# Kernel optimization log

Hardware: AMD Instinct MI355X
Metric: run time of the kernel (lower is better)

Reference implementation:

```python
import jax, jax.numpy as jnp
import numpy as np

B, T, D, H = 8, 4096, 512, 64

def setup_inputs() -> dict:
    key = jax.random.key(0)
    ks = jax.random.split(key, 6)
    s = 0.02  # small init scale so exp(K), exp(wbias) stay numerically tame
    return {
        "x": jax.random.normal(ks[0], (B, T, D), dtype=jnp.float32),
        "wq": jax.random.normal(ks[1], (H, D), dtype=jnp.float32) * s,
        "bq": jnp.zeros((H,), dtype=jnp.float32),
        "wk": jax.random.normal(ks[2], (H, D), dtype=jnp.float32) * s,
        "bk": jnp.zeros((H,), dtype=jnp.float32),
        "wv": jax.random.normal(ks[3], (H, D), dtype=jnp.float32) * s,
        "bv": jnp.zeros((H,), dtype=jnp.float32),
        "wp": jax.random.normal(ks[4], (D, H), dtype=jnp.float32) * s,
        "bp": jnp.zeros((D,), dtype=jnp.float32),
        "wbias": jax.random.normal(ks[5], (T, T), dtype=jnp.float32) * s,
    }

def reference(x, wq, bq, wk, bk, wv, bv, wp, bp, wbias):
    # Q, K, V projections: [B, T, H]
    Q = jnp.einsum('btd,hd->bth', x, wq) + bq
    K = jnp.einsum('btd,hd->bth', x, wk) + bk
    V = jnp.einsum('btd,hd->bth', x, wv) + bv
    ew = jnp.exp(wbias)              # [T, T], computed once
    eK = jnp.exp(K)                  # [B, T, H]
    num = jnp.einsum('ts,bsh->bth', ew, eK * V)
    den = jnp.einsum('ts,bsh->bth', ew, eK)
    Yt = jax.nn.sigmoid(Q) * (num / den)
    # output projection back to dim: [B, T, D]
    return jnp.einsum('bth,dh->btd', Yt, wp) + bp
```

## Files before the change

kernel.cpp:

```cpp
#include <hip/hip_runtime.h>
#include <math.h>

typedef _Float16 f16;
typedef __attribute__((ext_vector_type(8))) _Float16 f16x8;
typedef __attribute__((ext_vector_type(4))) _Float16 f16x4;
typedef __attribute__((ext_vector_type(4))) float f32x4;
typedef __attribute__((ext_vector_type(16))) float f32x16;

#define MFMA16(a, b, c) __builtin_amdgcn_mfma_f32_16x16x32_f16((a), (b), (c), 0, 0, 0)
#define MFMA32(a, b, c) __builtin_amdgcn_mfma_f32_32x32x16_f16((a), (b), (c), 0, 0, 0)

__device__ __forceinline__ void gld16(const f16* g, f16* l) {
  __builtin_amdgcn_global_load_lds(
      (const __attribute__((address_space(1))) unsigned int*)g,
      (__attribute__((address_space(3))) unsigned int*)l, 16, 0, 0);
}

__device__ __forceinline__ f16x8 pack8(const float* src) {
  float4 f0 = *(const float4*)src;
  float4 f1 = *(const float4*)(src + 4);
  f16x8 v;
  v[0] = (f16)f0.x; v[1] = (f16)f0.y; v[2] = (f16)f0.z; v[3] = (f16)f0.w;
  v[4] = (f16)f1.x; v[5] = (f16)f1.y; v[6] = (f16)f1.z; v[7] = (f16)f1.w;
  return v;
}

__global__ __launch_bounds__(256) void prep_ew(const float* __restrict__ wb,
                                               f16* __restrict__ ew) {
  const size_t stride = (size_t)gridDim.x * 256;
  const size_t total = (size_t)4096 * 4096 / 4;
  for (size_t i = (size_t)blockIdx.x * 256 + threadIdx.x; i < total; i += stride) {
    float4 f = ((const float4*)wb)[i];
    f16x4 o;
    o.x = (f16)expf(f.x); o.y = (f16)expf(f.y);
    o.z = (f16)expf(f.z); o.w = (f16)expf(f.w);
    ((f16x4*)ew)[i] = o;
  }
}

__global__ __launch_bounds__(256) void prep_w(const float* __restrict__ wq,
                                              const float* __restrict__ wk,
                                              const float* __restrict__ wv,
                                              const float* __restrict__ wp,
                                              f16* __restrict__ wqkvb,
                                              f16* __restrict__ wpb) {
  int i = blockIdx.x * 256 + threadIdx.x;
  wqkvb[i] = (f16)wk[i];
  wqkvb[32768 + i] = (f16)wv[i];
  wqkvb[65536 + i] = (f16)wq[i];
  wpb[i] = (f16)wp[i];
}

__global__ __launch_bounds__(256) void k1_qkv(const float* __restrict__ x,
                                              const f16* __restrict__ wqkvb,
                                              const float* __restrict__ bq,
                                              const float* __restrict__ bk,
                                              const float* __restrict__ bv,
                                              f16* __restrict__ sigQ,
                                              f16* __restrict__ XT) {
  __shared__ alignas(16) f16 sW[192 * 64];
  __shared__ alignas(16) f16 sX[64 * 64];
  const int tid = threadIdx.x;
  const int wave = tid >> 6, lane = tid & 63;
  const int m0 = blockIdx.x * 64;
  const int l15 = lane & 15;

  f32x4 accQ[4], accK[4], accV[4];
#pragma unroll
  for (int j = 0; j < 4; ++j) {
    accQ[j] = (f32x4){0.f, 0.f, 0.f, 0.f};
    accK[j] = (f32x4){0.f, 0.f, 0.f, 0.f};
    accV[j] = (f32x4){0.f, 0.f, 0.f, 0.f};
  }

  const int sc8 = tid & 7;
  const int wr8 = (tid >> 3) & 7;
  const int wcol = (sc8 ^ wr8) * 8;

  for (int ks = 0; ks < 512; ks += 64) {
#pragma unroll
    for (int q = 0; q < 6; ++q) {
      int r = q * 32 + (tid >> 3);
      gld16(wqkvb + (size_t)r * 512 + ks + wcol, &sW[r * 64 + sc8 * 8]);
    }
#pragma unroll
    for (int u = 0; u < 2; ++u) {
      int un = tid + u * 256;
      int r = un >> 3, c8 = un & 7;
      *(f16x8*)&sX[r * 64 + ((c8 ^ (r & 7)) * 8)] =
          pack8(x + (size_t)(m0 + r) * 512 + ks + c8 * 8);
    }
    __syncthreads();
#pragma unroll
    for (int kk = 0; kk < 2; ++kk) {
      const int c = kk * 4 + (lane >> 4);
      const int rK = wave * 16 + l15;
      const int rV = 64 + rK;
      f16x8 aK = *(const f16x8*)&sW[rK * 64 + ((c ^ (rK & 7)) * 8)];
      f16x8 aV = *(const f16x8*)&sW[rV * 64 + ((c ^ (rV & 7)) * 8)];
      f16x8 aQ = *(const f16x8*)&sX[rK * 64 + ((c ^ (rK & 7)) * 8)];
#pragma unroll
      for (int j = 0; j < 4; ++j) {
        const int rX = j * 16 + l15;
        const int rWq = 128 + j * 16 + l15;
        f16x8 bx = *(const f16x8*)&sX[rX * 64 + ((c ^ (rX & 7)) * 8)];
        f16x8 bw = *(const f16x8*)&sW[rWq * 64 + ((c ^ (rWq & 7)) * 8)];
        accK[j] = MFMA16(aK, bx, accK[j]);
        accV[j] = MFMA16(aV, bx, accV[j]);
        accQ[j] = MFMA16(aQ, bw, accQ[j]);
      }
    }
    __syncthreads();
  }
  const int b = m0 >> 12, t0 = m0 & 4095;
#pragma unroll
  for (int j = 0; j < 4; ++j) {
    const int h = j * 16 + l15;
    const float bqv = bq[h];
#pragma unroll
    for (int r = 0; r < 4; ++r) {
      const int m = m0 + wave * 16 + (lane >> 4) * 4 + r;
      const float v = accQ[j][r] + bqv;
      sigQ[(size_t)m * 64 + h] = (f16)(1.f / (1.f + expf(-v)));
    }
  }
#pragma unroll
  for (int r = 0; r < 4; ++r) {
    const int h = wave * 16 + (lane >> 4) * 4 + r;
    const float bkv = bk[h], bvv = bv[h];
    const size_t rowKV = (size_t)(b * 128 + h) * 4096;
    const size_t rowK = (size_t)(b * 128 + 64 + h) * 4096;
#pragma unroll
    for (int j = 0; j < 4; ++j) {
      const int t = t0 + j * 16 + l15;
      const float ek = expf(accK[j][r] + bkv);
      const float ev = accV[j][r] + bvv;
      XT[rowKV + t] = (f16)(ek * ev);
      XT[rowK + t] = (f16)ek;
    }
  }
}

__global__ __launch_bounds__(512) void k2_big(const f16* __restrict__ A,
                                              const f16* __restrict__ Bm,
                                              const f16* __restrict__ sigQ,
                                              f16* __restrict__ Yt) {
  __shared__ alignas(16) f16 sA[2][128 * 128];
  __shared__ alignas(16) f16 sB[2][128 * 128];
  const int tid = threadIdx.x;
  const int wave = tid >> 6, lane = tid & 63;
  const int kh = wave >> 2;
  const int wq = wave & 3;
  const int wr = wq >> 1, wc = wq & 1;
  const int bid = blockIdx.x;
  const int b = (bid >> 3) & 7;
  const int m0 = ((bid & 7) + 8 * (bid >> 6)) * 128;
  const f16* Bbase = Bm + (size_t)(b * 128) * 4096;

  const int srow = tid >> 4;
  const int sc16 = tid & 15;
  const int gcol = (sc16 ^ (srow & 15)) * 8;

  f32x16 acc[2][2];
#pragma unroll
  for (int i = 0; i < 2; ++i)
#pragma unroll
    for (int j = 0; j < 2; ++j)
#pragma unroll
      for (int r = 0; r < 16; ++r) acc[i][j][r] = 0.f;

#define K2_STAGE(buf, ks)                                                              \
  do {                                                                                 \
    _Pragma("unroll") for (int q = 0; q < 4; ++q) {                                    \
      int r = q * 32 + srow;                                                           \
      gld16(A + (size_t)(m0 + r) * 4096 + (ks) + gcol, &sA[buf][r * 128 + sc16 * 8]);  \
      gld16(Bbase + (size_t)r * 4096 + (ks) + gcol, &sB[buf][r * 128 + sc16 * 8]);     \
    }                                                                                  \
  } while (0)

  K2_STAGE(0, 0);
  K2_STAGE(1, 128);
  asm volatile("s_waitcnt vmcnt(8)" ::: "memory");
  __builtin_amdgcn_s_barrier();
  asm volatile("" ::: "memory");

  const int rA0 = wr * 64 + (lane & 31);
  const int rB0 = wc * 32 + (lane & 31);
  const int l15x = lane & 15;
  const int nk = 4096 / 128;
  for (int t = 0; t < nk; ++t) {
    const int buf = t & 1;
#pragma unroll
    for (int kk = 0; kk < 4; ++kk) {
      const int c = kh * 8 + kk * 2 + (lane >> 5);
      const int cx = (c ^ l15x) * 8;
      f16x8 a0 = *(const f16x8*)&sA[buf][rA0 * 128 + cx];
      f16x8 a1 = *(const f16x8*)&sA[buf][(rA0 + 32) * 128 + cx];
      f16x8 b0 = *(const f16x8*)&sB[buf][rB0 * 128 + cx];
      f16x8 b1 = *(const f16x8*)&sB[buf][(rB0 + 64) * 128 + cx];
      acc[0][0] = MFMA32(a0, b0, acc[0][0]);
      acc[0][1] = MFMA32(a0, b1, acc[0][1]);
      acc[1][0] = MFMA32(a1, b0, acc[1][0]);
      acc[1][1] = MFMA32(a1, b1, acc[1][1]);
    }
    if (t + 1 < nk) {
      asm volatile("s_waitcnt lgkmcnt(0)" ::: "memory");
      __builtin_amdgcn_s_barrier();
      asm volatile("" ::: "memory");
      if (t + 2 < nk) {
        K2_STAGE(buf, (t + 2) * 128);
        asm volatile("s_waitcnt vmcnt(8)" ::: "memory");
      } else {
        asm volatile("s_waitcnt vmcnt(0)" ::: "memory");
      }
      __builtin_amdgcn_s_barrier();
      asm volatile("" ::: "memory");
    }
  }
#undef K2_STAGE

  __syncthreads();
  float* red = (float*)sA;
  if (kh == 1) {
#pragma unroll
    for (int i = 0; i < 2; ++i)
#pragma unroll
      for (int j = 0; j < 2; ++j)
#pragma unroll
        for (int r = 0; r < 16; ++r)
          red[(((wq * 2 + i) * 2 + j) << 10) + (r << 6) + lane] = acc[i][j][r];
  }
  __syncthreads();
  if (kh == 0) {
#pragma unroll
    for (int i = 0; i < 2; ++i)
#pragma unroll
      for (int j = 0; j < 2; ++j)
#pragma unroll
        for (int r = 0; r < 16; ++r)
          acc[i][j][r] += red[(((wq * 2 + i) * 2 + j) << 10) + (r << 6) + lane];
    const int colh = wc * 32 + (lane & 31);
    const int rbase = (lane >> 5) * 4;
#pragma unroll
    for (int i = 0; i < 2; ++i) {
      const int tb = m0 + wr * 64 + i * 32;
#pragma unroll
      for (int r = 0; r < 16; ++r) {
        const int trow = tb + (r & 3) + 8 * (r >> 2) + rbase;
        const size_t mrow = (size_t)b * 4096 + trow;
        const float num = acc[i][0][r];
        const float den = acc[i][1][r];
        const float sq = (float)sigQ[mrow * 64 + colh];
        Yt[mrow * 64 + colh] = (f16)(sq * num / den);
      }
    }
  }
}

__global__ __launch_bounds__(256) void k4_out(const f16* __restrict__ Yt,
                                              const f16* __restrict__ wpb,
                                              const float* __restrict__ bp,
                                              float* __restrict__ out) {
  __shared__ alignas(16) f16 sA[128 * 64];
  __shared__ alignas(16) f16 sB[128 * 64];
  const int tid = threadIdx.x;
  const int wave = tid >> 6, lane = tid & 63;
  const int m0 = blockIdx.x * 128;
  const int n0 = blockIdx.y * 128;
  const int wm = (wave >> 1) * 64;
  const int wn = (wave & 1) * 64;
  const int l15 = lane & 15;
  const int sc8 = tid & 7;
  const int scol = (sc8 ^ ((tid >> 3) & 7)) * 8;

#pragma unroll
  for (int q = 0; q < 4; ++q) {
    int r = q * 32 + (tid >> 3);
    gld16(Yt + (size_t)(m0 + r) * 64 + scol, &sA[r * 64 + sc8 * 8]);
    gld16(wpb + (size_t)(n0 + r) * 64 + scol, &sB[r * 64 + sc8 * 8]);
  }
  __syncthreads();

  f32x4 acc[4][4];
#pragma unroll
  for (int i = 0; i < 4; ++i)
#pragma unroll
    for (int j = 0; j < 4; ++j) acc[i][j] = (f32x4){0.f, 0.f, 0.f, 0.f};

#pragma unroll
  for (int kk = 0; kk < 2; ++kk) {
    const int c = kk * 4 + (lane >> 4);
    f16x8 af[4], bfr[4];
#pragma unroll
    for (int i = 0; i < 4; ++i) {
      const int r = wm + i * 16 + l15;
      af[i] = *(const f16x8*)&sA[r * 64 + ((c ^ (r & 7)) * 8)];
    }
#pragma unroll
    for (int j = 0; j < 4; ++j) {
      const int r = wn + j * 16 + l15;
      bfr[j] = *(const f16x8*)&sB[r * 64 + ((c ^ (r & 7)) * 8)];
    }
#pragma unroll
    for (int i = 0; i < 4; ++i)
#pragma unroll
      for (int j = 0; j < 4; ++j) acc[i][j] = MFMA16(af[i], bfr[j], acc[i][j]);
  }

#pragma unroll
  for (int i = 0; i < 4; ++i) {
    const int row = m0 + wm + i * 16 + (lane >> 4) * 4;
#pragma unroll
    for (int j = 0; j < 4; ++j) {
      const int col = n0 + wn + j * 16 + l15;
      const float bpv = bp[col];
#pragma unroll
      for (int r = 0; r < 4; ++r)
        out[(size_t)(row + r) * 512 + col] = acc[i][j][r] + bpv;
    }
  }
}

extern "C" void kernel_launch(void* const* d_in, const int* in_sizes, int n_in,
                              void* d_out, int out_size, void* d_ws, size_t ws_size,
                              hipStream_t stream) {
  const float* x = (const float*)d_in[0];
  const float* wq = (const float*)d_in[1];
  const float* bq = (const float*)d_in[2];
  const float* wk = (const float*)d_in[3];
  const float* bk = (const float*)d_in[4];
  const float* wv = (const float*)d_in[5];
  const float* bv = (const float*)d_in[6];
  const float* wp = (const float*)d_in[7];
  const float* bp = (const float*)d_in[8];
  const float* wbias = (const float*)d_in[9];
  float* out = (float*)d_out;

  char* ws = (char*)d_ws;
  f16* ew = (f16*)(ws);
  f16* XT = (f16*)(ws + 33554432);
  f16* sigQ = (f16*)(ws + 41943040);
  f16* Yt = (f16*)(ws + 46137344);
  f16* wqkvb = (f16*)(ws + 50331648);
  f16* wpb = (f16*)(ws + 50528256);

  prep_ew<<<4096, 256, 0, stream>>>(wbias, ew);
  prep_w<<<128, 256, 0, stream>>>(wq, wk, wv, wp, wqkvb, wpb);
  k1_qkv<<<512, 256, 0, stream>>>(x, wqkvb, bq, bk, bv, sigQ, XT);
  k2_big<<<256, 512, 0, stream>>>(ew, XT, sigQ, Yt);
  k4_out<<<dim3(256, 4), 256, 0, stream>>>(Yt, wpb, bp, out);
}
```

Before: 97.30 us.

## Repartition k2 waves into four K-split groups with larger per-wave tiles

The 8 waves of the big T×T GEMM kernel are reorganised from a 2-way K split over 2x2 spatial tiles into a 4-way K split over 2 column halves. Each wave now covers 128x64 output with 4x2 32x32 MFMA accumulators, which raises MFMA work per LDS fragment load. Fragment loads are hoisted ahead of an s_setprio-raised MFMA block, and the partial sums are merged with a two-level reduction through shared memory. The doubled accumulator count raises register pressure (launch_bounds 512,2), and the final reduction needs extra barriers and LDS traffic.

```diff
diff --git a/kernel.cpp b/kernel.cpp
--- a/kernel.cpp
+++ b/kernel.cpp
@@ -141,17 +141,15 @@
   }
 }
 
-__global__ __launch_bounds__(512) void k2_big(const f16* __restrict__ A,
-                                              const f16* __restrict__ Bm,
-                                              const f16* __restrict__ sigQ,
-                                              f16* __restrict__ Yt) {
-  __shared__ alignas(16) f16 sA[2][128 * 128];
-  __shared__ alignas(16) f16 sB[2][128 * 128];
+__global__ __launch_bounds__(512, 2) void k2_big(const f16* __restrict__ A,
+                                                 const f16* __restrict__ Bm,
+                                                 const f16* __restrict__ sigQ,
+                                                 f16* __restrict__ Yt) {
+  __shared__ alignas(16) f16 smem[4][128 * 128];
   const int tid = threadIdx.x;
   const int wave = tid >> 6, lane = tid & 63;
-  const int kh = wave >> 2;
-  const int wq = wave & 3;
-  const int wr = wq >> 1, wc = wq & 1;
+  const int kq = wave >> 1;
+  const int ws = wave & 1;
   const int bid = blockIdx.x;
   const int b = (bid >> 3) & 7;
   const int m0 = ((bid & 7) + 8 * (bid >> 6)) * 128;
@@ -161,21 +159,23 @@
   const int sc16 = tid & 15;
   const int gcol = (sc16 ^ (srow & 15)) * 8;
 
-  f32x16 acc[2][2];
-#pragma unroll
-  for (int i = 0; i < 2; ++i)
+  f32x16 acc[4][2];
+#pragma unroll
+  for (int i = 0; i < 4; ++i)
 #pragma unroll
     for (int j = 0; j < 2; ++j)
 #pragma unroll
       for (int r = 0; r < 16; ++r) acc[i][j][r] = 0.f;
 
-#define K2_STAGE(buf, ks)                                                              \
-  do {                                                                                 \
-    _Pragma("unroll") for (int q = 0; q < 4; ++q) {                                    \
-      int r = q * 32 + srow;                                                           \
-      gld16(A + (size_t)(m0 + r) * 4096 + (ks) + gcol, &sA[buf][r * 128 + sc16 * 8]);  \
-      gld16(Bbase + (size_t)r * 4096 + (ks) + gcol, &sB[buf][r * 128 + sc16 * 8]);     \
-    }                                                                                  \
+#define K2_STAGE(buf, ks)                                                          \
+  do {                                                                             \
+    _Pragma("unroll") for (int q = 0; q < 4; ++q) {                                \
+      int r = q * 32 + srow;                                                       \
+      gld16(A + (size_t)(m0 + r) * 4096 + (ks) + gcol,                             \
+            &smem[buf][r * 128 + sc16 * 8]);                                       \
+      gld16(Bbase + (size_t)r * 4096 + (ks) + gcol,                                \
+            &smem[2 + (buf)][r * 128 + sc16 * 8]);                                 \
+    }                                                                              \
   } while (0)
 
   K2_STAGE(0, 0);
@@ -184,25 +184,36 @@
   __builtin_amdgcn_s_barrier();
   asm volatile("" ::: "memory");
 
-  const int rA0 = wr * 64 + (lane & 31);
-  const int rB0 = wc * 32 + (lane & 31);
-  const int l15x = lane & 15;
+  const int l31 = lane & 31, l15 = lane & 15, lhi = lane >> 5;
+  const int c0 = kq * 4 + lhi;
+  const int cx0 = (c0 ^ l15) * 8;
+  const int cx1 = ((c0 + 2) ^ l15) * 8;
   const int nk = 4096 / 128;
   for (int t = 0; t < nk; ++t) {
     const int buf = t & 1;
-#pragma unroll
-    for (int kk = 0; kk < 4; ++kk) {
-      const int c = kh * 8 + kk * 2 + (lane >> 5);
-      const int cx = (c ^ l15x) * 8;
-      f16x8 a0 = *(const f16x8*)&sA[buf][rA0 * 128 + cx];
-      f16x8 a1 = *(const f16x8*)&sA[buf][(rA0 + 32) * 128 + cx];
-      f16x8 b0 = *(const f16x8*)&sB[buf][rB0 * 128 + cx];
-      f16x8 b1 = *(const f16x8*)&sB[buf][(rB0 + 64) * 128 + cx];
-      acc[0][0] = MFMA32(a0, b0, acc[0][0]);
-      acc[0][1] = MFMA32(a0, b1, acc[0][1]);
-      acc[1][0] = MFMA32(a1, b0, acc[1][0]);
-      acc[1][1] = MFMA32(a1, b1, acc[1][1]);
-    }
+    const f16* pA = smem[buf];
+    const f16* pB = smem[2 + buf];
+    f16x8 a0[4], a1[4], b0[2], b1[2];
+#pragma unroll
+    for (int i = 0; i < 4; ++i) a0[i] = *(const f16x8*)&pA[(i * 32 + l31) * 128 + cx0];
+#pragma unroll
+    for (int j = 0; j < 2; ++j)
+      b0[j] = *(const f16x8*)&pB[(j * 64 + ws * 32 + l31) * 128 + cx0];
+#pragma unroll
+    for (int i = 0; i < 4; ++i) a1[i] = *(const f16x8*)&pA[(i * 32 + l31) * 128 + cx1];
+#pragma unroll
+    for (int j = 0; j < 2; ++j)
+      b1[j] = *(const f16x8*)&pB[(j * 64 + ws * 32 + l31) * 128 + cx1];
+    __builtin_amdgcn_s_setprio(1);
+#pragma unroll
+    for (int i = 0; i < 4; ++i)
+#pragma unroll
+      for (int j = 0; j < 2; ++j) acc[i][j] = MFMA32(a0[i], b0[j], acc[i][j]);
+#pragma unroll
+    for (int i = 0; i < 4; ++i)
+#pragma unroll
+      for (int j = 0; j < 2; ++j) acc[i][j] = MFMA32(a1[i], b1[j], acc[i][j]);
+    __builtin_amdgcn_s_setprio(0);
     if (t + 1 < nk) {
       asm volatile("s_waitcnt lgkmcnt(0)" ::: "memory");
       __builtin_amdgcn_s_barrier();
@@ -220,41 +231,56 @@
 #undef K2_STAGE
 
   __syncthreads();
-  float* red = (float*)sA;
-  if (kh == 1) {
-#pragma unroll
-    for (int i = 0; i < 2; ++i)
+  float* scr = (float*)smem;
+  const int rit0 = 4 * lhi;
+#define MRG_ADDR(reg, i, j, r) \
+  ((reg) * 16384 + ((i) * 32 + ((r) & 3) + 8 * ((r) >> 2) + rit0) * 128 + (j) * 64 + ws * 32 + l31)
+  if (kq & 1) {
+#pragma unroll
+    for (int i = 0; i < 4; ++i)
 #pragma unroll
       for (int j = 0; j < 2; ++j)
 #pragma unroll
-        for (int r = 0; r < 16; ++r)
-          red[(((wq * 2 + i) * 2 + j) << 10) + (r << 6) + lane] = acc[i][j][r];
-  }
-  __syncthreads();
-  if (kh == 0) {
-#pragma unroll
-    for (int i = 0; i < 2; ++i)
+        for (int r = 0; r < 16; ++r) scr[MRG_ADDR(kq >> 1, i, j, r)] = acc[i][j][r];
+  }
+  __syncthreads();
+  if (!(kq & 1)) {
+#pragma unroll
+    for (int i = 0; i < 4; ++i)
 #pragma unroll
       for (int j = 0; j < 2; ++j)
 #pragma unroll
-        for (int r = 0; r < 16; ++r)
-          acc[i][j][r] += red[(((wq * 2 + i) * 2 + j) << 10) + (r << 6) + lane];
-    const int colh = wc * 32 + (lane & 31);
-    const int rbase = (lane >> 5) * 4;
-#pragma unroll
-    for (int i = 0; i < 2; ++i) {
-      const int tb = m0 + wr * 64 + i * 32;
+        for (int r = 0; r < 16; ++r) acc[i][j][r] += scr[MRG_ADDR(kq >> 1, i, j, r)];
+  }
+  __syncthreads();
+  if (kq == 2) {
+#pragma unroll
+    for (int i = 0; i < 4; ++i)
+#pragma unroll
+      for (int j = 0; j < 2; ++j)
+#pragma unroll
+        for (int r = 0; r < 16; ++r) scr[MRG_ADDR(0, i, j, r)] = acc[i][j][r];
+  }
+  __syncthreads();
+  if (kq == 0) {
+#pragma unroll
+    for (int i = 0; i < 4; ++i)
+#pragma unroll
+      for (int j = 0; j < 2; ++j)
+#pragma unroll
+        for (int r = 0; r < 16; ++r) acc[i][j][r] += scr[MRG_ADDR(0, i, j, r)];
+    const int h = ws * 32 + l31;
+#pragma unroll
+    for (int i = 0; i < 4; ++i)
 #pragma unroll
       for (int r = 0; r < 16; ++r) {
-        const int trow = tb + (r & 3) + 8 * (r >> 2) + rbase;
+        const int trow = m0 + i * 32 + (r & 3) + 8 * (r >> 2) + rit0;
         const size_t mrow = (size_t)b * 4096 + trow;
-        const float num = acc[i][0][r];
-        const float den = acc[i][1][r];
-        const float sq = (float)sigQ[mrow * 64 + colh];
-        Yt[mrow * 64 + colh] = (f16)(sq * num / den);
+        const float sq = (float)sigQ[mrow * 64 + h];
+        Yt[mrow * 64 + h] = (f16)(sq * acc[i][0][r] / acc[i][1][r]);
       }
-    }
-  }
+  }
+#undef MRG_ADDR
 }
 
 __global__ __launch_bounds__(256) void k4_out(const f16* __restrict__ Yt,
```

Measured after the change: 99.63 us. 2.4% more time.

## Fuse exp(wbias) conversion into the big GEMM A-tile load path

Applied to the files above, without the earlier changes.

Removes the separate prep_ew kernel that materialised exp(wbias) as fp16, and instead loads fp32 wbias in the GEMM, applies fast exp in registers, and writes the swizzled fp16 tile to LDS. The B operand still uses direct global-to-LDS loads, with a restructured double-buffer pipeline that prefetches A two stages ahead into registers. This saves a kernel launch and the fp16 intermediate round trip. In exchange, each A tile is read in fp32 and exponentiated once per batch block, which doubles A-side bytes and adds register pressure.

```diff
diff --git a/kernel.cpp b/kernel.cpp
--- a/kernel.cpp
+++ b/kernel.cpp
@@ -23,19 +23,6 @@
   v[0] = (f16)f0.x; v[1] = (f16)f0.y; v[2] = (f16)f0.z; v[3] = (f16)f0.w;
   v[4] = (f16)f1.x; v[5] = (f16)f1.y; v[6] = (f16)f1.z; v[7] = (f16)f1.w;
   return v;
-}
-
-__global__ __launch_bounds__(256) void prep_ew(const float* __restrict__ wb,
-                                               f16* __restrict__ ew) {
-  const size_t stride = (size_t)gridDim.x * 256;
-  const size_t total = (size_t)4096 * 4096 / 4;
-  for (size_t i = (size_t)blockIdx.x * 256 + threadIdx.x; i < total; i += stride) {
-    float4 f = ((const float4*)wb)[i];
-    f16x4 o;
-    o.x = (f16)expf(f.x); o.y = (f16)expf(f.y);
-    o.z = (f16)expf(f.z); o.w = (f16)expf(f.w);
-    ((f16x4*)ew)[i] = o;
-  }
 }
 
 __global__ __launch_bounds__(256) void prep_w(const float* __restrict__ wq,
@@ -141,7 +128,7 @@
   }
 }
 
-__global__ __launch_bounds__(512) void k2_big(const f16* __restrict__ A,
+__global__ __launch_bounds__(512) void k2_big(const float* __restrict__ Ap,
                                               const f16* __restrict__ Bm,
                                               const f16* __restrict__ sigQ,
                                               f16* __restrict__ Yt) {
@@ -155,12 +142,15 @@
   const int bid = blockIdx.x;
   const int b = (bid >> 3) & 7;
   const int m0 = ((bid & 7) + 8 * (bid >> 6)) * 128;
-  const f16* Bbase = Bm + (size_t)(b * 128) * 4096;
+  const f16* Bb = Bm + (size_t)(b * 128) * 4096;
 
   const int srow = tid >> 4;
   const int sc16 = tid & 15;
   const int gcol = (sc16 ^ (srow & 15)) * 8;
 
+  const int ar = tid >> 2;
+  const int ac = (tid & 3) * 32;
+
   f32x16 acc[2][2];
 #pragma unroll
   for (int i = 0; i < 2; ++i)
@@ -169,55 +159,88 @@
 #pragma unroll
       for (int r = 0; r < 16; ++r) acc[i][j][r] = 0.f;
 
-#define K2_STAGE(buf, ks)                                                              \
-  do {                                                                                 \
-    _Pragma("unroll") for (int q = 0; q < 4; ++q) {                                    \
-      int r = q * 32 + srow;                                                           \
-      gld16(A + (size_t)(m0 + r) * 4096 + (ks) + gcol, &sA[buf][r * 128 + sc16 * 8]);  \
-      gld16(Bbase + (size_t)r * 4096 + (ks) + gcol, &sB[buf][r * 128 + sc16 * 8]);     \
-    }                                                                                  \
+  float4 An[8];
+
+#define K2_LOADA(ks)                                                            \
+  do {                                                                          \
+    const float* ap = Ap + (size_t)(m0 + ar) * 4096 + (ks) + ac;                \
+    _Pragma("unroll") for (int q = 0; q < 8; ++q) An[q] = *(const float4*)(ap + q * 4); \
   } while (0)
 
-  K2_STAGE(0, 0);
-  K2_STAGE(1, 128);
-  asm volatile("s_waitcnt vmcnt(8)" ::: "memory");
+#define K2_WRITEA(buf)                                                          \
+  do {                                                                          \
+    _Pragma("unroll") for (int h = 0; h < 4; ++h) {                             \
+      f16x8 v;                                                                  \
+      v[0] = (f16)__expf(An[2 * h].x);                                          \
+      v[1] = (f16)__expf(An[2 * h].y);                                          \
+      v[2] = (f16)__expf(An[2 * h].z);                                          \
+      v[3] = (f16)__expf(An[2 * h].w);                                          \
+      v[4] = (f16)__expf(An[2 * h + 1].x);                                      \
+      v[5] = (f16)__expf(An[2 * h + 1].y);                                      \
+      v[6] = (f16)__expf(An[2 * h + 1].z);                                      \
+      v[7] = (f16)__expf(An[2 * h + 1].w);                                      \
+      const int c = (tid & 3) * 4 + h;                                          \
+      *(f16x8*)&sA[buf][ar * 128 + ((c ^ (ar & 15)) * 8)] = v;                  \
+    }                                                                           \
+  } while (0)
+
+#define K2_STAGEB(buf, ks)                                                      \
+  do {                                                                          \
+    _Pragma("unroll") for (int q = 0; q < 4; ++q) {                             \
+      int r = q * 32 + srow;                                                    \
+      gld16(Bb + (size_t)r * 4096 + (ks) + gcol, &sB[buf][r * 128 + sc16 * 8]); \
+    }                                                                           \
+  } while (0)
+
+  K2_LOADA(0);
+  K2_STAGEB(0, 0);
+  K2_WRITEA(0);
+  K2_LOADA(128);
+  K2_STAGEB(1, 128);
+  K2_WRITEA(1);
+  asm volatile("s_waitcnt vmcnt(4)" ::: "memory");
+  asm volatile("s_waitcnt lgkmcnt(0)" ::: "memory");
+  __builtin_amdgcn_sched_barrier(0);
   __builtin_amdgcn_s_barrier();
-  asm volatile("" ::: "memory");
 
   const int rA0 = wr * 64 + (lane & 31);
   const int rB0 = wc * 32 + (lane & 31);
   const int l15x = lane & 15;
-  const int nk = 4096 / 128;
+  const int nk = 32;
   for (int t = 0; t < nk; ++t) {
-    const int buf = t & 1;
+    const int cur = t & 1;
+    if (t + 2 < nk) K2_LOADA((t + 2) * 128);
+    __builtin_amdgcn_sched_barrier(0);
 #pragma unroll
     for (int kk = 0; kk < 4; ++kk) {
       const int c = kh * 8 + kk * 2 + (lane >> 5);
       const int cx = (c ^ l15x) * 8;
-      f16x8 a0 = *(const f16x8*)&sA[buf][rA0 * 128 + cx];
-      f16x8 a1 = *(const f16x8*)&sA[buf][(rA0 + 32) * 128 + cx];
-      f16x8 b0 = *(const f16x8*)&sB[buf][rB0 * 128 + cx];
-      f16x8 b1 = *(const f16x8*)&sB[buf][(rB0 + 64) * 128 + cx];
+      f16x8 a0 = *(const f16x8*)&sA[cur][rA0 * 128 + cx];
+      f16x8 a1 = *(const f16x8*)&sA[cur][(rA0 + 32) * 128 + cx];
+      f16x8 b0 = *(const f16x8*)&sB[cur][rB0 * 128 + cx];
+      f16x8 b1 = *(const f16x8*)&sB[cur][(rB0 + 64) * 128 + cx];
       acc[0][0] = MFMA32(a0, b0, acc[0][0]);
       acc[0][1] = MFMA32(a0, b1, acc[0][1]);
       acc[1][0] = MFMA32(a1, b0, acc[1][0]);
       acc[1][1] = MFMA32(a1, b1, acc[1][1]);
     }
-    if (t + 1 < nk) {
+    asm volatile("s_waitcnt lgkmcnt(0)" ::: "memory");
+    __builtin_amdgcn_sched_barrier(0);
+    __builtin_amdgcn_s_barrier();
+    if (t + 2 < nk) {
+      K2_STAGEB(cur, (t + 2) * 128);
+      __builtin_amdgcn_sched_barrier(0);
+      K2_WRITEA(cur);
       asm volatile("s_waitcnt lgkmcnt(0)" ::: "memory");
-      __builtin_amdgcn_s_barrier();
-      asm volatile("" ::: "memory");
-      if (t + 2 < nk) {
-        K2_STAGE(buf, (t + 2) * 128);
-        asm volatile("s_waitcnt vmcnt(8)" ::: "memory");
-      } else {
-        asm volatile("s_waitcnt vmcnt(0)" ::: "memory");
-      }
-      __builtin_amdgcn_s_barrier();
-      asm volatile("" ::: "memory");
-    }
-  }
-#undef K2_STAGE
+    } else {
+      asm volatile("s_waitcnt vmcnt(0)" ::: "memory");
+    }
+    __builtin_amdgcn_sched_barrier(0);
+    __builtin_amdgcn_s_barrier();
+  }
+#undef K2_LOADA
+#undef K2_WRITEA
+#undef K2_STAGEB
 
   __syncthreads();
   float* red = (float*)sA;
@@ -337,16 +360,14 @@
   float* out = (float*)d_out;
 
   char* ws = (char*)d_ws;
-  f16* ew = (f16*)(ws);
-  f16* XT = (f16*)(ws + 33554432);
-  f16* sigQ = (f16*)(ws + 41943040);
-  f16* Yt = (f16*)(ws + 46137344);
-  f16* wqkvb = (f16*)(ws + 50331648);
-  f16* wpb = (f16*)(ws + 50528256);
-
-  prep_ew<<<4096, 256, 0, stream>>>(wbias, ew);
+  f16* XT = (f16*)(ws);
+  f16* sigQ = (f16*)(ws + 8388608);
+  f16* Yt = (f16*)(ws + 12582912);
+  f16* wqkvb = (f16*)(ws + 16777216);
+  f16* wpb = (f16*)(ws + 16973824);
+
   prep_w<<<128, 256, 0, stream>>>(wq, wk, wv, wp, wqkvb, wpb);
   k1_qkv<<<512, 256, 0, stream>>>(x, wqkvb, bq, bk, bv, sigQ, XT);
-  k2_big<<<256, 512, 0, stream>>>(ew, XT, sigQ, Yt);
+  k2_big<<<256, 512, 0, stream>>>(wbias, XT, sigQ, Yt);
   k4_out<<<dim3(256, 4), 256, 0, stream>>>(Yt, wpb, bp, out);
 }
```

After: 147.1 us. 51.2% more time.

## Retile k2 into 64-row split-free blocks with smaller K stages

Applied to the files above, without the earlier changes.

The main GEMM-like kernel moves from 512-thread blocks with 128x128 tiles and an intra-block split-K reduction to 256-thread blocks. Each block now covers 64 output rows, computes the numerator and denominator accumulators directly per wave, and steps K in chunks of 64. The aim is to double the block count for better CU occupancy, drop the shared-memory reduction epilogue, and shrink LDS use. s_setprio and sched_barrier are added around the MFMA section. The trade-off is that the XT operand is reloaded twice as often, which lowers arithmetic intensity per block.

```diff
diff --git a/kernel.cpp b/kernel.cpp
--- a/kernel.cpp
+++ b/kernel.cpp
@@ -141,119 +141,97 @@
   }
 }
 
-__global__ __launch_bounds__(512) void k2_big(const f16* __restrict__ A,
+__global__ __launch_bounds__(256) void k2_big(const f16* __restrict__ A,
                                               const f16* __restrict__ Bm,
                                               const f16* __restrict__ sigQ,
                                               f16* __restrict__ Yt) {
-  __shared__ alignas(16) f16 sA[2][128 * 128];
-  __shared__ alignas(16) f16 sB[2][128 * 128];
+  __shared__ alignas(16) f16 sA[2][32 * 128];
+  __shared__ alignas(16) f16 sB[2][64 * 128];
   const int tid = threadIdx.x;
   const int wave = tid >> 6, lane = tid & 63;
-  const int kh = wave >> 2;
-  const int wq = wave & 3;
-  const int wr = wq >> 1, wc = wq & 1;
+  const int wr = wave >> 1, wc = wave & 1;
   const int bid = blockIdx.x;
   const int b = (bid >> 3) & 7;
-  const int m0 = ((bid & 7) + 8 * (bid >> 6)) * 128;
-  const f16* Bbase = Bm + (size_t)(b * 128) * 4096;
-
-  const int srow = tid >> 4;
-  const int sc16 = tid & 15;
-  const int gcol = (sc16 ^ (srow & 15)) * 8;
-
-  f32x16 acc[2][2];
-#pragma unroll
-  for (int i = 0; i < 2; ++i)
-#pragma unroll
-    for (int j = 0; j < 2; ++j)
-#pragma unroll
-      for (int r = 0; r < 16; ++r) acc[i][j][r] = 0.f;
-
-#define K2_STAGE(buf, ks)                                                              \
-  do {                                                                                 \
-    _Pragma("unroll") for (int q = 0; q < 4; ++q) {                                    \
-      int r = q * 32 + srow;                                                           \
-      gld16(A + (size_t)(m0 + r) * 4096 + (ks) + gcol, &sA[buf][r * 128 + sc16 * 8]);  \
-      gld16(Bbase + (size_t)r * 4096 + (ks) + gcol, &sB[buf][r * 128 + sc16 * 8]);     \
-    }                                                                                  \
+  const int m0 = ((bid & 7) + 8 * (bid >> 6)) * 64;
+  const f16* Bb = Bm + (size_t)(b * 128) * 4096;
+
+  int aRow[2], aCol[2];
+#pragma unroll
+  for (int q = 0; q < 2; ++q) {
+    int d = q * 256 + tid;
+    int lrow = d >> 4, cc = d & 15;
+    int oc = cc ^ (lrow & 15);
+    aRow[q] = lrow + 32 * (oc >> 3);
+    aCol[q] = (oc & 7) * 8;
+  }
+  int bRow[4], bCol[4];
+#pragma unroll
+  for (int q = 0; q < 4; ++q) {
+    int d = q * 256 + tid;
+    int lrow = d >> 4, cc = d & 15;
+    int oc = cc ^ (lrow & 15);
+    bRow[q] = lrow + 64 * (oc >> 3);
+    bCol[q] = (oc & 7) * 8;
+  }
+
+  f32x16 accN, accD;
+#pragma unroll
+  for (int r = 0; r < 16; ++r) { accN[r] = 0.f; accD[r] = 0.f; }
+
+#define K2_STAGE(buf, ks)                                                          \
+  do {                                                                             \
+    _Pragma("unroll") for (int q = 0; q < 2; ++q)                                  \
+        gld16(A + (size_t)(m0 + aRow[q]) * 4096 + (ks) + aCol[q],                  \
+              &sA[buf][(q * 256 + tid) * 8]);                                      \
+    _Pragma("unroll") for (int q = 0; q < 4; ++q)                                  \
+        gld16(Bb + (size_t)bRow[q] * 4096 + (ks) + bCol[q],                        \
+              &sB[buf][(q * 256 + tid) * 8]);                                      \
   } while (0)
 
   K2_STAGE(0, 0);
-  K2_STAGE(1, 128);
-  asm volatile("s_waitcnt vmcnt(8)" ::: "memory");
+  K2_STAGE(1, 64);
+  asm volatile("s_waitcnt vmcnt(6)" ::: "memory");
+  __builtin_amdgcn_sched_barrier(0);
   __builtin_amdgcn_s_barrier();
-  asm volatile("" ::: "memory");
-
-  const int rA0 = wr * 64 + (lane & 31);
-  const int rB0 = wc * 32 + (lane & 31);
-  const int l15x = lane & 15;
-  const int nk = 4096 / 128;
+
+  const int l31 = lane & 31, l15 = lane & 15, lhi = lane >> 5;
+  const int nk = 64;
   for (int t = 0; t < nk; ++t) {
-    const int buf = t & 1;
+    const int cur = t & 1;
+    const f16* pA = sA[cur];
+    const f16* pB = sB[cur];
+    __builtin_amdgcn_s_setprio(1);
 #pragma unroll
     for (int kk = 0; kk < 4; ++kk) {
-      const int c = kh * 8 + kk * 2 + (lane >> 5);
-      const int cx = (c ^ l15x) * 8;
-      f16x8 a0 = *(const f16x8*)&sA[buf][rA0 * 128 + cx];
-      f16x8 a1 = *(const f16x8*)&sA[buf][(rA0 + 32) * 128 + cx];
-      f16x8 b0 = *(const f16x8*)&sB[buf][rB0 * 128 + cx];
-      f16x8 b1 = *(const f16x8*)&sB[buf][(rB0 + 64) * 128 + cx];
-      acc[0][0] = MFMA32(a0, b0, acc[0][0]);
-      acc[0][1] = MFMA32(a0, b1, acc[0][1]);
-      acc[1][0] = MFMA32(a1, b0, acc[1][0]);
-      acc[1][1] = MFMA32(a1, b1, acc[1][1]);
-    }
-    if (t + 1 < nk) {
-      asm volatile("s_waitcnt lgkmcnt(0)" ::: "memory");
-      __builtin_amdgcn_s_barrier();
-      asm volatile("" ::: "memory");
-      if (t + 2 < nk) {
-        K2_STAGE(buf, (t + 2) * 128);
-        asm volatile("s_waitcnt vmcnt(8)" ::: "memory");
-      } else {
-        asm volatile("s_waitcnt vmcnt(0)" ::: "memory");
-      }
-      __builtin_amdgcn_s_barrier();
-      asm volatile("" ::: "memory");
-    }
+      const int c = kk * 2 + lhi;
+      f16x8 af = *(const f16x8*)&pA[l31 * 128 + (((wr * 8 + c) ^ l15) * 8)];
+      f16x8 b0 = *(const f16x8*)&pB[(wc * 32 + l31) * 128 + ((c ^ l15) * 8)];
+      f16x8 b1 = *(const f16x8*)&pB[(wc * 32 + l31) * 128 + (((8 + c) ^ l15) * 8)];
+      accN = MFMA32(af, b0, accN);
+      accD = MFMA32(af, b1, accD);
+    }
+    __builtin_amdgcn_s_setprio(0);
+    asm volatile("s_waitcnt lgkmcnt(0)" ::: "memory");
+    __builtin_amdgcn_sched_barrier(0);
+    __builtin_amdgcn_s_barrier();
+    if (t + 2 < nk) {
+      K2_STAGE(cur, (t + 2) * 64);
+      asm volatile("s_waitcnt vmcnt(6)" ::: "memory");
+    } else {
+      asm volatile("s_waitcnt vmcnt(0)" ::: "memory");
+    }
+    __builtin_amdgcn_sched_barrier(0);
+    __builtin_amdgcn_s_barrier();
   }
 #undef K2_STAGE
 
-  __syncthreads();
-  float* red = (float*)sA;
-  if (kh == 1) {
-#pragma unroll
-    for (int i = 0; i < 2; ++i)
-#pragma unroll
-      for (int j = 0; j < 2; ++j)
-#pragma unroll
-        for (int r = 0; r < 16; ++r)
-          red[(((wq * 2 + i) * 2 + j) << 10) + (r << 6) + lane] = acc[i][j][r];
-  }
-  __syncthreads();
-  if (kh == 0) {
-#pragma unroll
-    for (int i = 0; i < 2; ++i)
-#pragma unroll
-      for (int j = 0; j < 2; ++j)
-#pragma unroll
-        for (int r = 0; r < 16; ++r)
-          acc[i][j][r] += red[(((wq * 2 + i) * 2 + j) << 10) + (r << 6) + lane];
-    const int colh = wc * 32 + (lane & 31);
-    const int rbase = (lane >> 5) * 4;
-#pragma unroll
-    for (int i = 0; i < 2; ++i) {
-      const int tb = m0 + wr * 64 + i * 32;
-#pragma unroll
-      for (int r = 0; r < 16; ++r) {
-        const int trow = tb + (r & 3) + 8 * (r >> 2) + rbase;
-        const size_t mrow = (size_t)b * 4096 + trow;
-        const float num = acc[i][0][r];
-        const float den = acc[i][1][r];
-        const float sq = (float)sigQ[mrow * 64 + colh];
-        Yt[mrow * 64 + colh] = (f16)(sq * num / den);
-      }
-    }
+  const int h = wc * 32 + l31;
+#pragma unroll
+  for (int r = 0; r < 16; ++r) {
+    const int trow = m0 + wr * 32 + (r & 3) + 8 * (r >> 2) + 4 * lhi;
+    const size_t mrow = (size_t)b * 4096 + trow;
+    const float sq = (float)sigQ[mrow * 64 + h];
+    Yt[mrow * 64 + h] = (f16)(sq * accN[r] / accD[r]);
   }
 }
 
@@ -347,6 +325,6 @@
   prep_ew<<<4096, 256, 0, stream>>>(wbias, ew);
   prep_w<<<128, 256, 0, stream>>>(wq, wk, wv, wp, wqkvb, wpb);
   k1_qkv<<<512, 256, 0, stream>>>(x, wqkvb, bq, bk, bv, sigQ, XT);
-  k2_big<<<256, 512, 0, stream>>>(ew, XT, sigQ, Yt);
+  k2_big<<<512, 256, 0, stream>>>(ew, XT, sigQ, Yt);
   k4_out<<<dim3(256, 4), 256, 0, stream>>>(Yt, wpb, bp, out);
 }
```

New measurement: 105.7 us. 8.6% more time.
